# Performance work log

Hardware: AMD Instinct MI355X
Metric: run time of the kernel (lower is better)

The kernel has to match this reference:

```python
import jax, jax.numpy as jnp
import numpy as np

G1 = 3.0      # cfg.TRAIN.IoU_Gamma1
G2 = 5.0      # cfg.TRAIN.IoU_Gamma2
THR = 0.05    # centerness gap threshold from original pair filter


def setup_inputs() -> dict:
    key = jax.random.key(0)
    ks = jax.random.split(key, 8)
    B, N = 8, 2048
    cls = jax.random.normal(ks[0], (B, N, 2), jnp.float32)
    label_cls = jax.random.normal(ks[1], (B, N), jnp.float32)
    label_loc = jax.random.uniform(ks[2], (B, 4, N), jnp.float32, 0.05, 1.0)
    xy1 = jax.random.uniform(ks[3], (B, 2, N), jnp.float32, 0.0, 0.5)
    wh = jax.random.uniform(ks[4], (B, 2, N), jnp.float32, 0.05, 0.5)
    pred_bboxes = jnp.concatenate([xy1, xy1 + wh], axis=1)  # (B,4,N) = x1,y1,x2,y2
    txy1 = jax.random.uniform(ks[5], (B, 2), jnp.float32, 0.0, 0.5)
    twh = jax.random.uniform(ks[6], (B, 2), jnp.float32, 0.05, 0.5)
    label_target = jnp.concatenate([txy1, txy1 + twh], axis=1)  # (B,4)
    return {"cls": cls, "label_cls": label_cls, "label_loc": label_loc,
            "pred_bboxes": pred_bboxes, "label_target": label_target,
            "flagsigmoid": 1}


def _iou_vs_target(pred_bboxes, label_target):
    # pred_bboxes (B,4,N), label_target (B,4) -> iou (B,N)
    x1, y1, x2, y2 = (pred_bboxes[:, k] for k in range(4))
    tx1, ty1, tx2, ty2 = (label_target[:, k:k + 1] for k in range(4))  # (B,1)
    ww = jnp.clip(jnp.minimum(tx2, x2) - jnp.maximum(tx1, x1), 0)
    hh = jnp.clip(jnp.minimum(ty2, y2) - jnp.maximum(ty1, y1), 0)
    area = (x2 - x1) * (y2 - y1)
    tarea = (tx2 - tx1) * (ty2 - ty1)
    inter = ww * hh
    return inter / (area + tarea - inter)


def reference(cls, label_cls, label_loc, pred_bboxes, label_target, flagsigmoid):
    B = label_cls.shape[0]
    label_cls = label_cls.reshape(B, -1)          # (B,N)
    label_loc = label_loc.reshape(B, 4, -1)       # (B,4,N)
    cls = cls.reshape(B, -1, 2)                   # (B,N,2)
    lr = label_loc[:, jnp.array([0, 2])]          # (B,2,N)
    tb = label_loc[:, jnp.array([1, 3])]
    centerness = jnp.sqrt((lr.min(axis=1) / lr.max(axis=1)) *
                          (tb.min(axis=1) / tb.max(axis=1)))  # (B,N)
    prob = cls[..., 1] if flagsigmoid else jnp.exp(cls[..., 1])  # (B,N)
    iou = _iou_vs_target(pred_bboxes, label_target)              # (B,N)

    pos = label_cls > 0                                          # (B,N)
    # pair (a,b) valid iff both positive and centerness[a] - centerness[b] > THR
    # (exactly the sorted double-loop pair set of the original)
    dc = centerness[:, :, None] - centerness[:, None, :]         # (B,N,N)
    mask = pos[:, :, None] & pos[:, None, :] & (dc > THR)
    cnt = mask.sum(axis=(1, 2)).astype(jnp.float32)              # (B,)

    e1 = jnp.where(mask, jnp.exp(-G1 * (prob[:, :, None] - prob[:, None, :])), 0.0)
    iou_d = jax.lax.stop_gradient(iou)
    e2 = jnp.where(mask, jnp.exp(-G2 * (iou[:, :, None] - iou_d[:, None, :])), 0.0)

    safe = jnp.maximum(cnt, 1.0)
    l1 = jnp.where(cnt > 0, e1.sum(axis=(1, 2)) / safe, 0.0)     # (B,)
    l2 = jnp.where(cnt > 0, e2.sum(axis=(1, 2)) / safe, 0.0)
    valid = (cnt > 0).astype(jnp.float32)
    nv = jnp.maximum(valid.sum(), 1.0)
    any_valid = valid.sum() > 0
    final1 = jnp.where(any_valid, (l1 * valid).sum() / nv, 0.0)
    final2 = jnp.where(any_valid, (l2 * valid).sum() / nv, 0.0)
    return (final1, final2)
```

## Files before the change

kernel.cpp:

```cpp
#include <hip/hip_runtime.h>
#include <math.h>

#define G1C 3.0f
#define G2C 5.0f
#define THRC 0.05f
#define BLK 256
#define IPT 4
#define JT  64

__device__ __forceinline__ void elem_vals(
    const float* __restrict__ cls, const float* __restrict__ label_cls,
    const float* __restrict__ label_loc, const float* __restrict__ pred,
    float tx1, float ty1, float tx2, float ty2,
    int b, int n, int N, int flag,
    float& c, float& prob, float& iou, bool& pos)
{
    const float* ll = label_loc + (size_t)b * 4 * N;
    float l  = ll[0 * N + n];
    float t  = ll[1 * N + n];
    float r  = ll[2 * N + n];
    float bo = ll[3 * N + n];
    float mnlr = fminf(l, r),  mxlr = fmaxf(l, r);
    float mntb = fminf(t, bo), mxtb = fmaxf(t, bo);
    c = sqrtf((mnlr / mxlr) * (mntb / mxtb));

    pos = label_cls[(size_t)b * N + n] > 0.0f;

    float p = cls[((size_t)b * N + n) * 2 + 1];
    prob = flag ? p : expf(p);

    const float* pb = pred + (size_t)b * 4 * N;
    float x1 = pb[0 * N + n], y1 = pb[1 * N + n];
    float x2 = pb[2 * N + n], y2 = pb[3 * N + n];
    float ww = fmaxf(fminf(tx2, x2) - fmaxf(tx1, x1), 0.0f);
    float hh = fmaxf(fminf(ty2, y2) - fmaxf(ty1, y1), 0.0f);
    float area  = (x2 - x1) * (y2 - y1);
    float tarea = (tx2 - tx1) * (ty2 - ty1);
    float inter = ww * hh;
    iou = inter / (area + tarea - inter);
}

__global__ __launch_bounds__(BLK) void pairwise_kernel(
    const float* __restrict__ cls, const float* __restrict__ label_cls,
    const float* __restrict__ label_loc, const float* __restrict__ pred,
    const float* __restrict__ tgt, const int* __restrict__ flagp,
    int N,
    double* __restrict__ part1, double* __restrict__ part2,
    unsigned int* __restrict__ partc)
{
    __shared__ float4 sJ[JT];
    __shared__ double w1[BLK / 64];
    __shared__ double w2[BLK / 64];
    __shared__ unsigned int wk[BLK / 64];

    const int b    = blockIdx.z;
    const int tid  = threadIdx.x;
    const int flag = *flagp;

    const float tx1 = tgt[b * 4 + 0], ty1 = tgt[b * 4 + 1];
    const float tx2 = tgt[b * 4 + 2], ty2 = tgt[b * 4 + 3];

    const int jbase = blockIdx.y * JT;
    if (tid < JT) {
        int j = jbase + tid;
        if (j < N) {
            float c, prob, iou; bool pos;
            elem_vals(cls, label_cls, label_loc, pred, tx1, ty1, tx2, ty2,
                      b, j, N, flag, c, prob, iou, pos);
            sJ[tid] = make_float4(pos ? c : INFINITY, expf(G1C * prob), expf(G2C * iou), 0.0f);
        } else {
            sJ[tid] = make_float4(INFINITY, 0.0f, 0.0f, 0.0f);
        }
    }

    float cthr[IPT], Ai[IPT], Ci[IPT];
    const int ibase = blockIdx.x * (BLK * IPT) + tid;
#pragma unroll
    for (int q = 0; q < IPT; ++q) {
        int i  = ibase + q * BLK;
        int ic = (i < N) ? i : (N - 1);
        float c, prob, iou; bool pos;
        elem_vals(cls, label_cls, label_loc, pred, tx1, ty1, tx2, ty2,
                  b, ic, N, flag, c, prob, iou, pos);
        Ai[q]   = expf(-G1C * prob);
        Ci[q]   = expf(-G2C * iou);
        cthr[q] = (pos && i < N) ? (c - THRC) : -INFINITY;
    }

    __syncthreads();

    float aB[IPT], aD[IPT];
    int   kc[IPT];
#pragma unroll
    for (int q = 0; q < IPT; ++q) { aB[q] = 0.0f; aD[q] = 0.0f; kc[q] = 0; }

#pragma unroll 8
    for (int t = 0; t < JT; ++t) {
        float4 v = sJ[t];
#pragma unroll
        for (int q = 0; q < IPT; ++q) {
            bool m = v.x < cthr[q];
            aB[q] += m ? v.y : 0.0f;
            aD[q] += m ? v.z : 0.0f;
            kc[q] += m ? 1 : 0;
        }
    }

    double s1 = 0.0, s2 = 0.0;
    int kk = 0;
#pragma unroll
    for (int q = 0; q < IPT; ++q) {
        s1 += (double)Ai[q] * (double)aB[q];
        s2 += (double)Ci[q] * (double)aD[q];
        kk += kc[q];
    }
#pragma unroll
    for (int off = 32; off >= 1; off >>= 1) {
        s1 += __shfl_down(s1, off, 64);
        s2 += __shfl_down(s2, off, 64);
        kk += __shfl_down(kk, off, 64);
    }
    const int wid = tid >> 6, lane = tid & 63;
    if (lane == 0) { w1[wid] = s1; w2[wid] = s2; wk[wid] = (unsigned int)kk; }
    __syncthreads();
    if (tid == 0) {
        double t1 = 0.0, t2 = 0.0; unsigned int tk = 0;
#pragma unroll
        for (int w = 0; w < BLK / 64; ++w) { t1 += w1[w]; t2 += w2[w]; tk += wk[w]; }
        int pidx = (b * gridDim.y + blockIdx.y) * gridDim.x + blockIdx.x;
        part1[pidx] = t1;
        part2[pidx] = t2;
        partc[pidx] = tk;
    }
}

__global__ void finalize_kernel(
    const double* __restrict__ part1, const double* __restrict__ part2,
    const unsigned int* __restrict__ partc,
    int B, int nper, float* __restrict__ out)
{
    __shared__ double l1s[32], l2s[32];
    __shared__ int    vld[32];
    const int b = threadIdx.x >> 6, lane = threadIdx.x & 63;
    double s1 = 0.0, s2 = 0.0;
    unsigned long long c = 0;
    if (b < B) {
        for (int t = lane; t < nper; t += 64) {
            int idx = b * nper + t;
            s1 += part1[idx];
            s2 += part2[idx];
            c  += partc[idx];
        }
    }
#pragma unroll
    for (int off = 32; off >= 1; off >>= 1) {
        s1 += __shfl_down(s1, off, 64);
        s2 += __shfl_down(s2, off, 64);
        c  += __shfl_down(c,  off, 64);
    }
    if (b < B && lane == 0) {
        l1s[b] = (c > 0) ? s1 / (double)c : 0.0;
        l2s[b] = (c > 0) ? s2 / (double)c : 0.0;
        vld[b] = (c > 0) ? 1 : 0;
    }
    __syncthreads();
    if (threadIdx.x == 0) {
        double f1 = 0.0, f2 = 0.0; int nv = 0;
        for (int bb = 0; bb < B; ++bb) { f1 += l1s[bb]; f2 += l2s[bb]; nv += vld[bb]; }
        if (nv > 0) {
            out[0] = (float)(f1 / (double)nv);
            out[1] = (float)(f2 / (double)nv);
        } else {
            out[0] = 0.0f;
            out[1] = 0.0f;
        }
    }
}

extern "C" void kernel_launch(void* const* d_in, const int* in_sizes, int n_in,
                              void* d_out, int out_size, void* d_ws, size_t ws_size,
                              hipStream_t stream) {
    const float* cls       = (const float*)d_in[0];
    const float* label_cls = (const float*)d_in[1];
    const float* label_loc = (const float*)d_in[2];
    const float* pred      = (const float*)d_in[3];
    const float* tgt       = (const float*)d_in[4];
    const int*   flagp     = (const int*)d_in[5];

    const int B = in_sizes[4] / 4;
    const int N = in_sizes[1] / B;

    const int gx = (N + BLK * IPT - 1) / (BLK * IPT);
    const int gy = (N + JT - 1) / JT;
    const int nper = gx * gy;
    const size_t npart = (size_t)B * nper;

    double* part1 = (double*)d_ws;
    double* part2 = part1 + npart;
    unsigned int* partc = (unsigned int*)(part2 + npart);

    float* out = (float*)d_out;

    dim3 grid(gx, gy, B);
    dim3 block(BLK);
    pairwise_kernel<<<grid, block, 0, stream>>>(
        cls, label_cls, label_loc, pred, tgt, flagp, N, part1, part2, partc);
    finalize_kernel<<<1, 64 * B, 0, stream>>>(part1, part2, partc, B, nper, out);
}
```

Before: 17.44 us.

## Fuse finalize into pairwise kernel via last-block atomic and retile pair blocks

Merges the separate finalize kernel into the pairwise kernel, so the last block to finish (found through an atomic counter plus threadfence) performs the per-batch and global reductions. The pair tiling changes to 256 i by 128 j per block: per-element values are staged in shared memory and each thread handles 4 i values against a strided quarter of the j values. Precise divisions and exps become fast intrinsics. The aim is to save a kernel launch and raise block count, at the cost of an extra memset launch, more redundant per-element work across blocks, and slightly lower precision.

```diff
diff --git a/kernel.cpp b/kernel.cpp
--- a/kernel.cpp
+++ b/kernel.cpp
@@ -4,9 +4,9 @@
 #define G1C 3.0f
 #define G2C 5.0f
 #define THRC 0.05f
-#define BLK 256
-#define IPT 4
-#define JT  64
+#define BLK  256
+#define IBLK 256
+#define JBLK 128
 
 __device__ __forceinline__ void elem_vals(
     const float* __restrict__ cls, const float* __restrict__ label_cls,
@@ -22,12 +22,12 @@
     float bo = ll[3 * N + n];
     float mnlr = fminf(l, r),  mxlr = fmaxf(l, r);
     float mntb = fminf(t, bo), mxtb = fmaxf(t, bo);
-    c = sqrtf((mnlr / mxlr) * (mntb / mxtb));
+    c = sqrtf(__fdividef(mnlr, mxlr) * __fdividef(mntb, mxtb));
 
     pos = label_cls[(size_t)b * N + n] > 0.0f;
 
     float p = cls[((size_t)b * N + n) * 2 + 1];
-    prob = flag ? p : expf(p);
+    prob = flag ? p : __expf(p);
 
     const float* pb = pred + (size_t)b * 4 * N;
     float x1 = pb[0 * N + n], y1 = pb[1 * N + n];
@@ -37,68 +37,75 @@
     float area  = (x2 - x1) * (y2 - y1);
     float tarea = (tx2 - tx1) * (ty2 - ty1);
     float inter = ww * hh;
-    iou = inter / (area + tarea - inter);
+    iou = __fdividef(inter, area + tarea - inter);
 }
 
-__global__ __launch_bounds__(BLK) void pairwise_kernel(
+__global__ __launch_bounds__(BLK) void fused_kernel(
     const float* __restrict__ cls, const float* __restrict__ label_cls,
     const float* __restrict__ label_loc, const float* __restrict__ pred,
     const float* __restrict__ tgt, const int* __restrict__ flagp,
-    int N,
+    int N, int B, int nblk,
     double* __restrict__ part1, double* __restrict__ part2,
-    unsigned int* __restrict__ partc)
+    unsigned int* __restrict__ partc,
+    unsigned int* __restrict__ counter, float* __restrict__ out)
 {
-    __shared__ float4 sJ[JT];
-    __shared__ double w1[BLK / 64];
-    __shared__ double w2[BLK / 64];
+    __shared__ float4 sI[IBLK];
+    __shared__ float4 sJ[JBLK];
+    __shared__ double w1[BLK / 64], w2[BLK / 64];
     __shared__ unsigned int wk[BLK / 64];
-
+    __shared__ int isLast;
+    __shared__ double l1s[32], l2s[32];
+    __shared__ int vld[32];
+
+    const int tid  = threadIdx.x;
     const int b    = blockIdx.z;
-    const int tid  = threadIdx.x;
     const int flag = *flagp;
 
     const float tx1 = tgt[b * 4 + 0], ty1 = tgt[b * 4 + 1];
     const float tx2 = tgt[b * 4 + 2], ty2 = tgt[b * 4 + 3];
 
-    const int jbase = blockIdx.y * JT;
-    if (tid < JT) {
+    const int ibase = blockIdx.x * IBLK;
+    {
+        int i = ibase + tid;
+        if (i < N) {
+            float c, prob, iou; bool pos;
+            elem_vals(cls, label_cls, label_loc, pred, tx1, ty1, tx2, ty2,
+                      b, i, N, flag, c, prob, iou, pos);
+            sI[tid] = make_float4(pos ? (c - THRC) : -INFINITY,
+                                  __expf(-G1C * prob), __expf(-G2C * iou), 0.0f);
+        } else {
+            sI[tid] = make_float4(-INFINITY, 0.0f, 0.0f, 0.0f);
+        }
+    }
+    const int jbase = blockIdx.y * JBLK;
+    if (tid < JBLK) {
         int j = jbase + tid;
         if (j < N) {
             float c, prob, iou; bool pos;
             elem_vals(cls, label_cls, label_loc, pred, tx1, ty1, tx2, ty2,
                       b, j, N, flag, c, prob, iou, pos);
-            sJ[tid] = make_float4(pos ? c : INFINITY, expf(G1C * prob), expf(G2C * iou), 0.0f);
+            sJ[tid] = make_float4(pos ? c : INFINITY,
+                                  __expf(G1C * prob), __expf(G2C * iou), 0.0f);
         } else {
             sJ[tid] = make_float4(INFINITY, 0.0f, 0.0f, 0.0f);
         }
     }
-
-    float cthr[IPT], Ai[IPT], Ci[IPT];
-    const int ibase = blockIdx.x * (BLK * IPT) + tid;
-#pragma unroll
-    for (int q = 0; q < IPT; ++q) {
-        int i  = ibase + q * BLK;
-        int ic = (i < N) ? i : (N - 1);
-        float c, prob, iou; bool pos;
-        elem_vals(cls, label_cls, label_loc, pred, tx1, ty1, tx2, ty2,
-                  b, ic, N, flag, c, prob, iou, pos);
-        Ai[q]   = expf(-G1C * prob);
-        Ci[q]   = expf(-G2C * iou);
-        cthr[q] = (pos && i < N) ? (c - THRC) : -INFINITY;
-    }
-
     __syncthreads();
 
-    float aB[IPT], aD[IPT];
-    int   kc[IPT];
-#pragma unroll
-    for (int q = 0; q < IPT; ++q) { aB[q] = 0.0f; aD[q] = 0.0f; kc[q] = 0; }
-
-#pragma unroll 8
-    for (int t = 0; t < JT; ++t) {
-        float4 v = sJ[t];
-#pragma unroll
-        for (int q = 0; q < IPT; ++q) {
+    const int il = tid >> 2, jl = tid & 3;
+    float cthr[4], Ai[4], Ci[4];
+#pragma unroll
+    for (int q = 0; q < 4; ++q) {
+        float4 v = sI[(il << 2) + q];
+        cthr[q] = v.x; Ai[q] = v.y; Ci[q] = v.z;
+    }
+    float aB[4] = {0.f, 0.f, 0.f, 0.f}, aD[4] = {0.f, 0.f, 0.f, 0.f};
+    int   kc[4] = {0, 0, 0, 0};
+#pragma unroll
+    for (int t = 0; t < JBLK / 4; ++t) {
+        float4 v = sJ[(t << 2) + jl];
+#pragma unroll
+        for (int q = 0; q < 4; ++q) {
             bool m = v.x < cthr[q];
             aB[q] += m ? v.y : 0.0f;
             aD[q] += m ? v.z : 0.0f;
@@ -109,7 +116,7 @@
     double s1 = 0.0, s2 = 0.0;
     int kk = 0;
 #pragma unroll
-    for (int q = 0; q < IPT; ++q) {
+    for (int q = 0; q < 4; ++q) {
         s1 += (double)Ai[q] * (double)aB[q];
         s2 += (double)Ci[q] * (double)aD[q];
         kk += kc[q];
@@ -123,56 +130,57 @@
     const int wid = tid >> 6, lane = tid & 63;
     if (lane == 0) { w1[wid] = s1; w2[wid] = s2; wk[wid] = (unsigned int)kk; }
     __syncthreads();
+
+    const int nper = gridDim.x * gridDim.y;
     if (tid == 0) {
         double t1 = 0.0, t2 = 0.0; unsigned int tk = 0;
 #pragma unroll
         for (int w = 0; w < BLK / 64; ++w) { t1 += w1[w]; t2 += w2[w]; tk += wk[w]; }
-        int pidx = (b * gridDim.y + blockIdx.y) * gridDim.x + blockIdx.x;
+        int pidx = b * nper + blockIdx.y * gridDim.x + blockIdx.x;
         part1[pidx] = t1;
         part2[pidx] = t2;
         partc[pidx] = tk;
-    }
-}
-
-__global__ void finalize_kernel(
-    const double* __restrict__ part1, const double* __restrict__ part2,
-    const unsigned int* __restrict__ partc,
-    int B, int nper, float* __restrict__ out)
-{
-    __shared__ double l1s[32], l2s[32];
-    __shared__ int    vld[32];
-    const int b = threadIdx.x >> 6, lane = threadIdx.x & 63;
-    double s1 = 0.0, s2 = 0.0;
-    unsigned long long c = 0;
-    if (b < B) {
-        for (int t = lane; t < nper; t += 64) {
-            int idx = b * nper + t;
-            s1 += part1[idx];
-            s2 += part2[idx];
-            c  += partc[idx];
-        }
-    }
-#pragma unroll
-    for (int off = 32; off >= 1; off >>= 1) {
-        s1 += __shfl_down(s1, off, 64);
-        s2 += __shfl_down(s2, off, 64);
-        c  += __shfl_down(c,  off, 64);
-    }
-    if (b < B && lane == 0) {
-        l1s[b] = (c > 0) ? s1 / (double)c : 0.0;
-        l2s[b] = (c > 0) ? s2 / (double)c : 0.0;
-        vld[b] = (c > 0) ? 1 : 0;
+        __threadfence();
+        unsigned int old = atomicAdd(counter, 1u);
+        isLast = (old == (unsigned int)(nblk - 1)) ? 1 : 0;
     }
     __syncthreads();
-    if (threadIdx.x == 0) {
-        double f1 = 0.0, f2 = 0.0; int nv = 0;
-        for (int bb = 0; bb < B; ++bb) { f1 += l1s[bb]; f2 += l2s[bb]; nv += vld[bb]; }
-        if (nv > 0) {
-            out[0] = (float)(f1 / (double)nv);
-            out[1] = (float)(f2 / (double)nv);
-        } else {
-            out[0] = 0.0f;
-            out[1] = 0.0f;
+
+    if (isLast) {
+        __threadfence();
+        const int w = tid >> 6, nw = BLK / 64;
+        for (int bb = w; bb < B; bb += nw) {
+            double s1b = 0.0, s2b = 0.0;
+            unsigned long long c = 0;
+            for (int t = lane; t < nper; t += 64) {
+                int idx = bb * nper + t;
+                s1b += part1[idx];
+                s2b += part2[idx];
+                c   += partc[idx];
+            }
+#pragma unroll
+            for (int off = 32; off >= 1; off >>= 1) {
+                s1b += __shfl_down(s1b, off, 64);
+                s2b += __shfl_down(s2b, off, 64);
+                c   += __shfl_down(c,   off, 64);
+            }
+            if (lane == 0) {
+                l1s[bb] = (c > 0) ? s1b / (double)c : 0.0;
+                l2s[bb] = (c > 0) ? s2b / (double)c : 0.0;
+                vld[bb] = (c > 0) ? 1 : 0;
+            }
+        }
+        __syncthreads();
+        if (tid == 0) {
+            double f1 = 0.0, f2 = 0.0; int nv = 0;
+            for (int bb = 0; bb < B; ++bb) { f1 += l1s[bb]; f2 += l2s[bb]; nv += vld[bb]; }
+            if (nv > 0) {
+                out[0] = (float)(f1 / (double)nv);
+                out[1] = (float)(f2 / (double)nv);
+            } else {
+                out[0] = 0.0f;
+                out[1] = 0.0f;
+            }
         }
     }
 }
@@ -190,20 +198,23 @@
     const int B = in_sizes[4] / 4;
     const int N = in_sizes[1] / B;
 
-    const int gx = (N + BLK * IPT - 1) / (BLK * IPT);
-    const int gy = (N + JT - 1) / JT;
-    const int nper = gx * gy;
-    const size_t npart = (size_t)B * nper;
-
-    double* part1 = (double*)d_ws;
+    const int gx = (N + IBLK - 1) / IBLK;
+    const int gy = (N + JBLK - 1) / JBLK;
+    const int nblk = gx * gy * B;
+    const size_t npart = (size_t)B * gx * gy;
+
+    unsigned int* counter = (unsigned int*)d_ws;
+    double* part1 = (double*)((char*)d_ws + 64);
     double* part2 = part1 + npart;
     unsigned int* partc = (unsigned int*)(part2 + npart);
 
     float* out = (float*)d_out;
 
+    hipMemsetAsync(counter, 0, sizeof(unsigned int), stream);
+
     dim3 grid(gx, gy, B);
     dim3 block(BLK);
-    pairwise_kernel<<<grid, block, 0, stream>>>(
-        cls, label_cls, label_loc, pred, tgt, flagp, N, part1, part2, partc);
-    finalize_kernel<<<1, 64 * B, 0, stream>>>(part1, part2, partc, B, nper, out);
+    fused_kernel<<<grid, block, 0, stream>>>(
+        cls, label_cls, label_loc, pred, tgt, flagp, N, B, nblk,
+        part1, part2, partc, counter, out);
 }
```

Measured after the change: 38.83 us. 123% more time.
